# Performance work log

Measured on AMD Instinct MI355X. Metric: run time of the kernel, lower is better.

## Reference

```python
import jax, jax.numpy as jnp
import numpy as np

H = 64       # hidden size hard-coded in the module
NH = 4       # n_heads
S = 500      # stock_num
D = 10       # num_day
T = 40       # num_text (news per day)
FP = 3       # price features
FT = 512     # text embedding dim


def gru_scan(x, Wih, Whh, bih, bhh):
    """Single-sequence GRU (torch gate convention). x: (T, F) -> hidden states (T, H)."""
    gi = x @ Wih + bih  # (T, 3H) precompute input gates outside the scan

    def step(h, g):
        gh = h @ Whh + bhh
        r = jax.nn.sigmoid(g[:H] + gh[:H])
        z = jax.nn.sigmoid(g[H:2 * H] + gh[H:2 * H])
        n = jnp.tanh(g[2 * H:] + r * gh[2 * H:])
        h_new = (1.0 - z) * n + z * h
        return h_new, h_new

    h0 = jnp.zeros((H,), x.dtype)
    _, hs = jax.lax.scan(step, h0, gi)
    return hs


def attn_pool(hs, W, v):
    """Additive attention pooling over time. hs: (T, H) -> (H,)."""
    scores = jnp.tanh(hs @ W) @ v          # (T,)
    alpha = jax.nn.softmax(scores)
    return alpha @ hs


def _gru_params(key, fin, scale=0.08):
    k1, k2, k3, k4 = jax.random.split(key, 4)
    return (jax.random.normal(k1, (S, fin, 3 * H)) * scale,
            jax.random.normal(k2, (S, H, 3 * H)) * scale,
            jax.random.normal(k3, (S, 3 * H)) * scale,
            jax.random.normal(k4, (S, 3 * H)) * scale)


def _attn_params(key, scale=0.08):
    k1, k2 = jax.random.split(key)
    return (jax.random.normal(k1, (S, H, H)) * scale,
            jax.random.normal(k2, (S, H)) * scale)


def setup_inputs() -> dict:
    key = jax.random.key(0)
    ks = jax.random.split(key, 20)
    inp = {}
    inp['text_input'] = jax.random.normal(ks[0], (S, D, T, FT), dtype=jnp.float32)
    inp['price_input'] = jax.random.normal(ks[1], (S, D, FP), dtype=jnp.float32)
    inp['label'] = jax.random.randint(ks[2], (S,), 0, 2)
    inp['adj'] = jnp.ones((S, S), dtype=jnp.float32)
    inp['train'] = 0
    # per-stock stacked parameters
    (inp['Wih_p'], inp['Whh_p'], inp['bih_p'], inp['bhh_p']) = _gru_params(ks[3], FP)
    (inp['Wa_p'], inp['va_p']) = _attn_params(ks[4])
    (inp['Wih_t'], inp['Whh_t'], inp['bih_t'], inp['bhh_t']) = _gru_params(ks[5], FT)
    (inp['Wa_t'], inp['va_t']) = _attn_params(ks[6])
    (inp['Wih_s'], inp['Whh_s'], inp['bih_s'], inp['bhh_s']) = _gru_params(ks[7], H)
    (inp['Wa_s'], inp['va_s']) = _attn_params(ks[8])
    inp['Wb'] = jax.random.normal(ks[9], (S, H, H, H)) * 0.05   # Bilinear weight (out,in1,in2)
    inp['bb'] = jax.random.normal(ks[10], (S, H)) * 0.05
    inp['Wbl'] = jax.random.normal(ks[11], (S, H, 2)) * 0.08
    inp['bbl'] = jax.random.normal(ks[12], (S, 2)) * 0.08
    # shared cross-stock self-attention projections and final fc
    inp['Wq'] = jax.random.normal(ks[13], (H, H)) * 0.08
    inp['bq'] = jax.random.normal(ks[14], (H,)) * 0.08
    inp['Wk'] = jax.random.normal(ks[15], (H, H)) * 0.08
    inp['bk'] = jax.random.normal(ks[16], (H,)) * 0.08
    inp['Wf'] = jax.random.normal(ks[17], (H, 2)) * 0.08
    inp['bf'] = jax.random.normal(ks[18], (2,)) * 0.08
    return inp


def _forward(text_input, price_input, label,
             Wih_p, Whh_p, bih_p, bhh_p, Wa_p, va_p,
             Wih_t, Whh_t, bih_t, bhh_t, Wa_t, va_t,
             Wih_s, Whh_s, bih_s, bhh_s, Wa_s, va_s,
             Wb, bb, Wbl, bbl, Wq, bq, Wk, bk, Wf, bf):
    # ---- per-stock price encoder: GRU over days + attention pooling ----
    def enc_price(x, a, b, c, d, W, v):
        return attn_pool(gru_scan(x, a, b, c, d), W, v)
    x_price = jax.vmap(enc_price)(price_input, Wih_p, Whh_p, bih_p, bhh_p, Wa_p, va_p)  # (S, H)

    # ---- per-stock, per-day text encoder ----
    def enc_text_stock(xdays, a, b, c, d, W, v):
        return jax.vmap(lambda x: attn_pool(gru_scan(x, a, b, c, d), W, v))(xdays)  # (D, H)
    news = jax.vmap(enc_text_stock)(text_input, Wih_t, Whh_t, bih_t, bhh_t, Wa_t, va_t)  # (S, D, H)

    # ---- per-stock sequence encoder over days ----
    text_vec = jax.vmap(enc_price)(news, Wih_s, Whh_s, bih_s, bhh_s, Wa_s, va_s)  # (S, H)

    # ---- bilinear fusion: tanh(Bilinear(text, price)) ----
    combined = jnp.tanh(jnp.einsum('si,skij,sj->sk', text_vec, Wb, x_price) + bb)  # (S, H)

    # ---- per-stock blending head ----
    out_1 = jnp.tanh(jnp.einsum('si,sik->sk', combined, Wbl) + bbl)  # (S, 2)

    # ---- cross-stock multi-head self-attention (q,k projected, v identity) ----
    dh = H // NH
    q = (combined @ Wq + bq).reshape(S, NH, dh)
    k = (combined @ Wk + bk).reshape(S, NH, dh)
    v = combined.reshape(S, NH, dh)
    scores = jnp.einsum('shd,thd->hst', q, k) / (dh ** 0.5)
    attn = jax.nn.softmax(scores, axis=-1)
    attn_out = jnp.einsum('hst,thd->shd', attn, v).reshape(S, H)

    x = jax.nn.elu(attn_out @ Wf + bf)  # (S, 2)
    output = jax.nn.softmax(x + out_1, axis=1)
    # faithful to the original: CrossEntropyLoss applied to already-softmaxed output
    logp = jax.nn.log_softmax(output, axis=1)
    loss = -jnp.mean(logp[jnp.arange(S), label])
    return loss, output


def reference(text_input, price_input, label, adj, train,
              Wih_p, Whh_p, bih_p, bhh_p, Wa_p, va_p,
              Wih_t, Whh_t, bih_t, bhh_t, Wa_t, va_t,
              Wih_s, Whh_s, bih_s, bhh_s, Wa_s, va_s,
              Wb, bb, Wbl, bbl, Wq, bq, Wk, bk, Wf, bf):
    return _forward(text_input, price_input, label,
                    Wih_p, Whh_p, bih_p, bhh_p, Wa_p, va_p,
                    Wih_t, Whh_t, bih_t, bhh_t, Wa_t, va_t,
                    Wih_s, Whh_s, bih_s, bhh_s, Wa_s, va_s,
                    Wb, bb, Wbl, bbl, Wq, bq, Wk, bk, Wf, bf)
```

## Files before the change

### kernel.cpp

```cpp
#include <hip/hip_runtime.h>

#define Sn 500
#define Dn 10
#define Tn 40
#define FPn 3
#define FTn 512
#define Hn 64
#define G3 192
#define NHn 4

typedef __attribute__((ext_vector_type(8))) short bf8_t;
typedef __attribute__((ext_vector_type(4))) float f4_t;

__device__ __forceinline__ unsigned short f2bf(float f) {
    union { float f; unsigned int u; } v; v.f = f;
    unsigned int r = v.u + 0x7fffu + ((v.u >> 16) & 1u);
    return (unsigned short)(r >> 16);
}
__device__ __forceinline__ float bflo(unsigned int u) {
    union { unsigned int u; float f; } v; v.u = u << 16; return v.f;
}
__device__ __forceinline__ float bfhi(unsigned int u) {
    union { unsigned int u; float f; } v; v.u = u & 0xffff0000u; return v.f;
}
__device__ __forceinline__ unsigned int cvtpk(float lo, float hi) {
    unsigned int r;
    asm("v_cvt_pk_bf16_f32 %0, %1, %2" : "=v"(r) : "v"(lo), "v"(hi));
    return r;
}
__device__ __forceinline__ float sigmoidf_(float x) { return 1.f / (1.f + __expf(-x)); }
__device__ __forceinline__ float tanhf_(float x) {
    x = fminf(15.f, fmaxf(-15.f, x));
    float e = __expf(2.f * x);
    return (e - 1.f) / (e + 1.f);
}
__device__ __forceinline__ float dot8(uint4 wv, f4_t hA, f4_t hB) {
    return bflo(wv.x) * hA[0] + bfhi(wv.x) * hA[1]
         + bflo(wv.y) * hA[2] + bfhi(wv.y) * hA[3]
         + bflo(wv.z) * hB[0] + bfhi(wv.z) * hB[1]
         + bflo(wv.w) * hB[2] + bfhi(wv.w) * hB[3];
}
union bfu { bf8_t v; unsigned int u[4]; };

__global__ __launch_bounds__(64, 1) void price_gru(
    const float* __restrict__ price, const float* __restrict__ Wih_p,
    const float* __restrict__ Whh_p, const float* __restrict__ bih_p,
    const float* __restrict__ bhh_p, const float* __restrict__ Wa_p,
    const float* __restrict__ va_p, float* __restrict__ xprice)
{
    __shared__ __align__(16) unsigned char smp[33160];
    unsigned char* whh2 = smp;
    unsigned char* wa2 = smp + 24576;
    float* hbuf = (float*)(smp + 32768);
    float* priceL = (float*)(smp + 33040);

    const int s = blockIdx.x, l = threadIdx.x;
    {
        const float* W3 = Whh_p + (size_t)s * Hn * G3;
        for (int r = 0; r < 192; ++r) {
            int e = l + r * 64, i = e / G3, j = e - i * G3;
            *(unsigned short*)(whh2 + j * 128 + ((2 * i) ^ ((j & 7) << 4))) = f2bf(W3[e]);
        }
        const float* A3 = Wa_p + (size_t)s * Hn * Hn;
        for (int r = 0; r < 64; ++r) {
            int e = l + r * 64, i = e >> 6, k = e & 63;
            *(unsigned short*)(wa2 + k * 128 + ((2 * i) ^ ((k & 7) << 4))) = f2bf(A3[e]);
        }
        if (l < 30) priceL[l] = price[(size_t)s * 30 + l];
        hbuf[l] = 0.f;
        if (l < 4) hbuf[64 + l] = 0.f;
    }
    __builtin_amdgcn_wave_barrier();
    {
        float wp[3][3];
        #pragma unroll
        for (int i = 0; i < 3; ++i)
            #pragma unroll
            for (int g = 0; g < 3; ++g)
                wp[i][g] = Wih_p[(size_t)s * 3 * G3 + i * G3 + g * 64 + l];
        const float bi0 = bih_p[(size_t)s * G3 + l];
        const float bi1 = bih_p[(size_t)s * G3 + 64 + l];
        const float bi2 = bih_p[(size_t)s * G3 + 128 + l];
        const float bh0 = bhh_p[(size_t)s * G3 + l];
        const float bh1 = bhh_p[(size_t)s * G3 + 64 + l];
        const float bh2 = bhh_p[(size_t)s * G3 + 128 + l];
        const float vak = va_p[(size_t)s * Hn + l];
        const int swl = (l & 7) << 4;
        float h3 = 0.f, m3 = -1e30f, den3 = 0.f, av3 = 0.f;
        for (int t = 0; t < Dn; ++t) {
            float x0 = priceL[t * 3], x1 = priceL[t * 3 + 1], x2 = priceL[t * 3 + 2];
            float gg0 = bi0 + x0 * wp[0][0] + x1 * wp[1][0] + x2 * wp[2][0];
            float gg1 = bi1 + x0 * wp[0][1] + x1 * wp[1][1] + x2 * wp[2][1];
            float gg2 = bi2 + x0 * wp[0][2] + x1 * wp[1][2] + x2 * wp[2][2];
            float gh0 = bh0, gh1 = bh1, gh2 = bh2;
            #pragma unroll
            for (int ic = 0; ic < 8; ++ic) {
                const int off = (ic * 16) ^ swl;
                f4_t hA = *(const f4_t*)&hbuf[ic * 8];
                f4_t hB = *(const f4_t*)&hbuf[ic * 8 + 4];
                uint4 w0 = *(const uint4*)(whh2 + l * 128 + off);
                uint4 w1 = *(const uint4*)(whh2 + (l + 64) * 128 + off);
                uint4 w2 = *(const uint4*)(whh2 + (l + 128) * 128 + off);
                gh0 += dot8(w0, hA, hB); gh1 += dot8(w1, hA, hB); gh2 += dot8(w2, hA, hB);
            }
            float r = sigmoidf_(gg0 + gh0);
            float z = sigmoidf_(gg1 + gh1);
            float n = tanhf_(gg2 + r * gh2);
            h3 = (1.f - z) * n + z * h3;
            __builtin_amdgcn_wave_barrier();
            hbuf[l] = h3;
            __builtin_amdgcn_wave_barrier();
            float sk = 0.f;
            #pragma unroll
            for (int ic = 0; ic < 8; ++ic) {
                const int off = (ic * 16) ^ swl;
                uint4 wv = *(const uint4*)(wa2 + l * 128 + off);
                f4_t hA = *(const f4_t*)&hbuf[ic * 8];
                f4_t hB = *(const f4_t*)&hbuf[ic * 8 + 4];
                sk += dot8(wv, hA, hB);
            }
            float term = tanhf_(sk) * vak;
            #pragma unroll
            for (int off = 32; off; off >>= 1) term += __shfl_xor(term, off);
            float mn = fmaxf(m3, term);
            float s0 = __expf(m3 - mn);
            float p = __expf(term - mn);
            den3 = den3 * s0 + p;
            av3 = av3 * s0 + p * h3;
            m3 = mn;
        }
        xprice[(size_t)s * Hn + l] = av3 / den3;
    }
}

__global__ __launch_bounds__(256) void mega_fused(
    const float* __restrict__ text, const float* __restrict__ Wih,
    const float* __restrict__ bih, float* __restrict__ gi2,
    const float* __restrict__ Wb, const float* __restrict__ xprice,
    float* __restrict__ u)
{
    __shared__ __align__(16) unsigned char sm[20480];

    const int bid = blockIdx.x;
    const int xcd = bid & 7, ix = bid >> 3;
    const int swz = (xcd < 4 ? xcd * 813 : 3252 + (xcd - 4) * 812) + ix;
    const int grp = swz / 13, sub = swz - grp * 13;
    const int tid = threadIdx.x, w = tid >> 6, l = tid & 63;

    if (sub < 5) {
        const int s = grp, fi = sub;
        const int lr = l & 15, kg = l >> 4;
        unsigned short* Ab0 = (unsigned short*)sm;
        unsigned short* Ab1 = Ab0 + 5120;

        const float* xbase = text + ((size_t)s * 400 + fi * 80) * FTn;
        const float* Wihs = Wih + (size_t)s * FTn * G3 + w * 48 + lr;

        f4_t acc[5][3];
        #pragma unroll
        for (int a = 0; a < 5; a++)
            #pragma unroll
            for (int b = 0; b < 3; b++) acc[a][b] = (f4_t){0.f, 0.f, 0.f, 0.f};

        f4_t pa[3], pb[3];
        auto aload = [&](int kk) {
            #pragma unroll
            for (int q = 0; q < 3; ++q) {
                int c = tid + q * 256;
                if (q < 2 || tid < 128) {
                    int row = c >> 3, slot = c & 7;
                    const float* p = xbase + (size_t)row * FTn + kk * 64 + slot * 8;
                    pa[q] = *(const f4_t*)p; pb[q] = *(const f4_t*)(p + 4);
                }
            }
        };
        auto awrite = [&](unsigned short* buf) {
            #pragma unroll
            for (int q = 0; q < 3; ++q) {
                int c = tid + q * 256;
                if (q < 2 || tid < 128) {
                    int row = c >> 3, slot = c & 7;
                    uint4 uu = { cvtpk(pa[q][0], pa[q][1]), cvtpk(pa[q][2], pa[q][3]),
                                 cvtpk(pb[q][0], pb[q][1]), cvtpk(pb[q][2], pb[q][3]) };
                    *(uint4*)(buf + row * 64 + ((slot ^ (row & 7)) * 8)) = uu;
                }
            }
        };
        auto bload = [&](int kk, int ks, int nc) -> bf8_t {
            const float* bp = Wihs + (size_t)(kk * 64 + ks * 32 + kg * 8) * G3 + nc * 16;
            float b0 = bp[0], b1 = bp[G3], b2 = bp[2 * G3], b3 = bp[3 * G3];
            float b4 = bp[4 * G3], b5 = bp[5 * G3], b6 = bp[6 * G3], b7 = bp[7 * G3];
            bfu t;
            t.u[0] = cvtpk(b0, b1); t.u[1] = cvtpk(b2, b3);
            t.u[2] = cvtpk(b4, b5); t.u[3] = cvtpk(b6, b7);
            return t.v;
        };
        auto afrag = [&](const unsigned short* buf, int mt, int ks) -> bf8_t {
            int row = mt * 16 + lr;
            int slot = (ks * 4 + kg) ^ (row & 7);
            return *(const bf8_t*)(buf + row * 64 + slot * 8);
        };

        bf8_t bc[2][3], bn[2][3];
        aload(0);
        #pragma unroll
        for (int ks = 0; ks < 2; ++ks)
            #pragma unroll
            for (int nc = 0; nc < 3; ++nc) bc[ks][nc] = bload(0, ks, nc);
        awrite(Ab0);
        __syncthreads();

        for (int kk = 0; kk < 8; ++kk) {
            unsigned short* cur = (kk & 1) ? Ab1 : Ab0;
            unsigned short* nxt = (kk & 1) ? Ab0 : Ab1;
            if (kk < 7) {
                aload(kk + 1);
                #pragma unroll
                for (int ks = 0; ks < 2; ++ks)
                    #pragma unroll
                    for (int nc = 0; nc < 3; ++nc) bn[ks][nc] = bload(kk + 1, ks, nc);
            }
            #pragma unroll
            for (int ks = 0; ks < 2; ++ks)
                #pragma unroll
                for (int mt = 0; mt < 5; ++mt) {
                    bf8_t af = afrag(cur, mt, ks);
                    acc[mt][0] = __builtin_amdgcn_mfma_f32_16x16x32_bf16(af, bc[ks][0], acc[mt][0], 0, 0, 0);
                    acc[mt][1] = __builtin_amdgcn_mfma_f32_16x16x32_bf16(af, bc[ks][1], acc[mt][1], 0, 0, 0);
                    acc[mt][2] = __builtin_amdgcn_mfma_f32_16x16x32_bf16(af, bc[ks][2], acc[mt][2], 0, 0, 0);
                }
            if (kk < 7) awrite(nxt);
            __syncthreads();
            #pragma unroll
            for (int ks = 0; ks < 2; ++ks)
                #pragma unroll
                for (int nc = 0; nc < 3; ++nc) bc[ks][nc] = bn[ks][nc];
        }

        const float* bihs = bih + (size_t)s * G3 + w * 48 + lr;
        #pragma unroll
        for (int nc = 0; nc < 3; ++nc) {
            const int col = w * 48 + nc * 16 + lr;
            const float bv = bihs[nc * 16];
            #pragma unroll
            for (int mt = 0; mt < 5; ++mt)
                #pragma unroll
                for (int rg = 0; rg < 4; ++rg) {
                    int r = mt * 16 + kg * 4 + rg;
                    int hi = (r >= 40);
                    int day = fi * 2 + hi;
                    int t = r - hi * 40;
                    gi2[((size_t)(s * 40 + t) * 10 + day) * 192 + col] = acc[mt][nc][rg] + bv;
                }
        }
    } else {
        const int s = grp, kq = sub - 5;
        float* uT = (float*)sm;
        const int j4 = (l & 15) * 4;
        f4_t xq = *(const f4_t*)&xprice[s * Hn + j4];

        const float* Wbs = Wb + (size_t)s * Hn * Hn * Hn;
        for (int g = 0; g < 32; ++g) {
            int P = kq * 512 + g * 16 + w * 4 + (l >> 4);
            f4_t wv = *(const f4_t*)&Wbs[(size_t)P * Hn + j4];
            float dp = wv[0] * xq[0] + wv[1] * xq[1] + wv[2] * xq[2] + wv[3] * xq[3];
            dp += __shfl_xor(dp, 8);
            dp += __shfl_xor(dp, 4);
            dp += __shfl_xor(dp, 2);
            dp += __shfl_xor(dp, 1);
            if ((l & 15) == 0) { int k = P >> 6, i = P & 63; uT[i * 9 + (k - kq * 8)] = dp; }
        }
        __syncthreads();
        #pragma unroll
        for (int r = 0; r < 2; ++r) {
            int flat = tid + r * 256;
            int kL = flat >> 6, i = flat & 63;
            u[((size_t)s * 64 + kq * 8 + kL) * 64 + i] = uT[i * 9 + kL];
        }
    }
}

__global__ __launch_bounds__(64, 1) void gru_text_f(
    const float* __restrict__ gi2, const float* __restrict__ Whh,
    const float* __restrict__ bhh, const float* __restrict__ Wa,
    const float* __restrict__ va, float* __restrict__ news)
{
    __shared__ __align__(16) float hrow[16 * 68];
    __shared__ __align__(16) unsigned char waT[Hn * 128];

    const int s = blockIdx.x, l = threadIdx.x;
    const int lr = l & 15, lg = l >> 4;

    const float* Whhs = Whh + (size_t)s * Hn * G3;
    bfu bwhh[2][12];
    #pragma unroll
    for (int ks = 0; ks < 2; ++ks)
        #pragma unroll
        for (int nt = 0; nt < 12; ++nt) {
            const float* p = Whhs + (size_t)(ks * 32 + lg * 8) * G3 + nt * 16 + lr;
            float b0 = p[0], b1 = p[G3], b2 = p[2 * G3], b3 = p[3 * G3];
            float b4 = p[4 * G3], b5 = p[5 * G3], b6 = p[6 * G3], b7 = p[7 * G3];
            bwhh[ks][nt].u[0] = cvtpk(b0, b1); bwhh[ks][nt].u[1] = cvtpk(b2, b3);
            bwhh[ks][nt].u[2] = cvtpk(b4, b5); bwhh[ks][nt].u[3] = cvtpk(b6, b7);
        }
    float bhh_l[12];
    #pragma unroll
    for (int nt = 0; nt < 12; ++nt) bhh_l[nt] = bhh[(size_t)s * G3 + nt * 16 + lr];
    float va_l[4];
    #pragma unroll
    for (int nt = 0; nt < 4; ++nt) va_l[nt] = va[(size_t)s * Hn + nt * 16 + lr];

    {
        const float* Was = Wa + (size_t)s * Hn * Hn;
        for (int r = 0; r < 64; ++r) {
            int e = l + r * 64, i = e >> 6, k = e & 63;
            *(unsigned short*)(waT + k * 128 + ((2 * i) ^ ((k & 7) << 4))) = f2bf(Was[e]);
        }
        #pragma unroll
        for (int r = 0; r < 17; ++r) hrow[l + r * 64] = 0.f;
    }
    __builtin_amdgcn_wave_barrier();

    int dayoff[4];
    #pragma unroll
    for (int rr = 0; rr < 4; ++rr) {
        int d = lg * 4 + rr; if (d > 9) d = 9;
        dayoff[rr] = d * 192 + lr;
    }
    const float* gbase = gi2 + (size_t)s * 40 * 1920;

    float val[48], valn[48];
    #pragma unroll
    for (int j = 0; j < 48; ++j) val[j] = gbase[dayoff[j & 3] + (j >> 2) * 16];

    bf8_t a0f, a1f;
    {   bfu z0; z0.u[0] = 0; z0.u[1] = 0; z0.u[2] = 0; z0.u[3] = 0; a0f = z0.v; a1f = z0.v; }

    float h[4][4], accv[4][4], den[4], m[4];
    #pragma unroll
    for (int nt = 0; nt < 4; ++nt)
        #pragma unroll
        for (int rr = 0; rr < 4; ++rr) { h[nt][rr] = 0.f; accv[nt][rr] = 0.f; }
    #pragma unroll
    for (int rr = 0; rr < 4; ++rr) { den[rr] = 0.f; m[rr] = -1e30f; }

    for (int t = 0; t < Tn; ++t) {
        f4_t acc[12];
        #pragma unroll
        for (int nt = 0; nt < 12; ++nt)
            acc[nt] = (f4_t){bhh_l[nt], bhh_l[nt], bhh_l[nt], bhh_l[nt]};
        __builtin_amdgcn_s_setprio(1);
        #pragma unroll
        for (int nt = 0; nt < 12; ++nt) {
            acc[nt] = __builtin_amdgcn_mfma_f32_16x16x32_bf16(a0f, bwhh[0][nt].v, acc[nt], 0, 0, 0);
            acc[nt] = __builtin_amdgcn_mfma_f32_16x16x32_bf16(a1f, bwhh[1][nt].v, acc[nt], 0, 0, 0);
        }
        __builtin_amdgcn_s_setprio(0);
        {
            const int tn = (t < Tn - 1) ? t + 1 : t;
            const float* gb = gbase + (size_t)tn * 1920;
            #pragma unroll
            for (int j = 0; j < 48; ++j) valn[j] = gb[dayoff[j & 3] + (j >> 2) * 16];
        }
        #pragma unroll
        for (int nt = 0; nt < 4; ++nt)
            #pragma unroll
            for (int rr = 0; rr < 4; ++rr) {
                float r = sigmoidf_(val[nt * 4 + rr] + acc[nt][rr]);
                float z = sigmoidf_(val[(nt + 4) * 4 + rr] + acc[nt + 4][rr]);
                float n = tanhf_(val[(nt + 8) * 4 + rr] + r * acc[nt + 8][rr]);
                h[nt][rr] = (1.f - z) * n + z * h[nt][rr];
            }
        __builtin_amdgcn_wave_barrier();
        #pragma unroll
        for (int rr = 0; rr < 4; ++rr) {
            int day = lg * 4 + rr;
            if (day < Dn) {
                #pragma unroll
                for (int nt = 0; nt < 4; ++nt) hrow[day * 68 + nt * 16 + lr] = h[nt][rr];
            }
        }
        __builtin_amdgcn_wave_barrier();
        {
            const float* hp = hrow + lr * 68 + lg * 8;
            f4_t x0 = *(const f4_t*)hp,        x1 = *(const f4_t*)(hp + 4);
            f4_t y0 = *(const f4_t*)(hp + 32), y1 = *(const f4_t*)(hp + 36);
            bfu t0, t1;
            t0.u[0] = cvtpk(x0[0], x0[1]); t0.u[1] = cvtpk(x0[2], x0[3]);
            t0.u[2] = cvtpk(x1[0], x1[1]); t0.u[3] = cvtpk(x1[2], x1[3]);
            t1.u[0] = cvtpk(y0[0], y0[1]); t1.u[1] = cvtpk(y0[2], y0[3]);
            t1.u[2] = cvtpk(y1[0], y1[1]); t1.u[3] = cvtpk(y1[2], y1[3]);
            a0f = t0.v; a1f = t1.v;
        }
        f4_t sc[4];
        #pragma unroll
        for (int nt = 0; nt < 4; ++nt) sc[nt] = (f4_t){0.f, 0.f, 0.f, 0.f};
        __builtin_amdgcn_s_setprio(1);
        #pragma unroll
        for (int ks = 0; ks < 2; ++ks) {
            bf8_t av = ks ? a1f : a0f;
            #pragma unroll
            for (int nt = 0; nt < 4; ++nt) {
                bf8_t bwv = *(const bf8_t*)(waT + (nt * 16 + lr) * 128
                                            + ((ks * 64 + lg * 16) ^ ((lr & 7) << 4)));
                sc[nt] = __builtin_amdgcn_mfma_f32_16x16x32_bf16(av, bwv, sc[nt], 0, 0, 0);
            }
        }
        __builtin_amdgcn_s_setprio(0);
        float pr[4];
        #pragma unroll
        for (int rr = 0; rr < 4; ++rr) {
            pr[rr] = tanhf_(sc[0][rr]) * va_l[0] + tanhf_(sc[1][rr]) * va_l[1]
                   + tanhf_(sc[2][rr]) * va_l[2] + tanhf_(sc[3][rr]) * va_l[3];
            pr[rr] += __shfl_xor(pr[rr], 1);
            pr[rr] += __shfl_xor(pr[rr], 2);
            pr[rr] += __shfl_xor(pr[rr], 4);
            pr[rr] += __shfl_xor(pr[rr], 8);
        }
        #pragma unroll
        for (int rr = 0; rr < 4; ++rr) {
            float mn = fmaxf(m[rr], pr[rr]);
            float s0 = __expf(m[rr] - mn);
            float p = __expf(pr[rr] - mn);
            den[rr] = den[rr] * s0 + p;
            #pragma unroll
            for (int nt = 0; nt < 4; ++nt)
                accv[nt][rr] = accv[nt][rr] * s0 + p * h[nt][rr];
            m[rr] = mn;
        }
        #pragma unroll
        for (int j = 0; j < 48; ++j) val[j] = valn[j];
    }
    #pragma unroll
    for (int rr = 0; rr < 4; ++rr) {
        int day = lg * 4 + rr;
        if (day < Dn) {
            float inv = 1.f / den[rr];
            #pragma unroll
            for (int nt = 0; nt < 4; ++nt)
                news[((size_t)s * Dn + day) * Hn + nt * 16 + lr] = accv[nt][rr] * inv;
        }
    }
}

__global__ __launch_bounds__(64, 1) void day_finish(
    const float* __restrict__ news,
    const float* __restrict__ Wih_s, const float* __restrict__ Whh_s,
    const float* __restrict__ bih_s, const float* __restrict__ bhh_s,
    const float* __restrict__ Wa_s, const float* __restrict__ va_s,
    const float* __restrict__ u, const float* __restrict__ bb,
    const float* __restrict__ Wq, const float* __restrict__ bq,
    const float* __restrict__ Wk, const float* __restrict__ bk,
    const float* __restrict__ Wbl, const float* __restrict__ bbl,
    float* __restrict__ combined, float* __restrict__ qg,
    float* __restrict__ kg, float* __restrict__ out1)
{
    __shared__ __align__(16) unsigned char sm[60928];
    unsigned char* whh2 = sm;
    unsigned char* wih2 = sm + 24576;
    unsigned char* wa2 = sm + 49152;
    float* newsL = (float*)(sm + 57600);
    float* hbuf  = (float*)(sm + 60320);

    const int s = blockIdx.x, l = threadIdx.x;
    float tvv;

    {
        const float* W2 = Whh_s + (size_t)s * Hn * G3;
        const float* X2 = Wih_s + (size_t)s * Hn * G3;
        for (int r = 0; r < 192; ++r) {
            int e = l + r * 64, i = e / G3, j = e - i * G3;
            int off = j * 128 + ((2 * i) ^ ((j & 7) << 4));
            *(unsigned short*)(whh2 + off) = f2bf(W2[e]);
            *(unsigned short*)(wih2 + off) = f2bf(X2[e]);
        }
        const float* A2 = Wa_s + (size_t)s * Hn * Hn;
        for (int r = 0; r < 64; ++r) {
            int e = l + r * 64, i = e >> 6, k = e & 63;
            *(unsigned short*)(wa2 + k * 128 + ((2 * i) ^ ((k & 7) << 4))) = f2bf(A2[e]);
        }
        #pragma unroll
        for (int d = 0; d < Dn; ++d) newsL[d * 68 + l] = news[((size_t)s * Dn + d) * Hn + l];
        hbuf[l] = 0.f;
        if (l < 4) hbuf[64 + l] = 0.f;
    }
    __builtin_amdgcn_wave_barrier();
    {
        const float bi0 = bih_s[(size_t)s * G3 + l];
        const float bi1 = bih_s[(size_t)s * G3 + 64 + l];
        const float bi2 = bih_s[(size_t)s * G3 + 128 + l];
        const float bh0 = bhh_s[(size_t)s * G3 + l];
        const float bh1 = bhh_s[(size_t)s * G3 + 64 + l];
        const float bh2 = bhh_s[(size_t)s * G3 + 128 + l];
        const float vak = va_s[(size_t)s * Hn + l];
        const int swl = (l & 7) << 4;
        float h2 = 0.f, m2 = -1e30f, den2 = 0.f, av2 = 0.f;
        for (int t = 0; t < Dn; ++t) {
            float gh0 = bh0, gh1 = bh1, gh2 = bh2;
            float gg0 = bi0, gg1 = bi1, gg2 = bi2;
            #pragma unroll
            for (int ic = 0; ic < 8; ++ic) {
                const int off = (ic * 16) ^ swl;
                f4_t hA = *(const f4_t*)&hbuf[ic * 8];
                f4_t hB = *(const f4_t*)&hbuf[ic * 8 + 4];
                f4_t nA = *(const f4_t*)&newsL[t * 68 + ic * 8];
                f4_t nB = *(const f4_t*)&newsL[t * 68 + ic * 8 + 4];
                uint4 w0 = *(const uint4*)(whh2 + l * 128 + off);
                uint4 w1 = *(const uint4*)(whh2 + (l + 64) * 128 + off);
                uint4 w2 = *(const uint4*)(whh2 + (l + 128) * 128 + off);
                uint4 x0 = *(const uint4*)(wih2 + l * 128 + off);
                uint4 x1 = *(const uint4*)(wih2 + (l + 64) * 128 + off);
                uint4 x2 = *(const uint4*)(wih2 + (l + 128) * 128 + off);
                gh0 += dot8(w0, hA, hB); gh1 += dot8(w1, hA, hB); gh2 += dot8(w2, hA, hB);
                gg0 += dot8(x0, nA, nB); gg1 += dot8(x1, nA, nB); gg2 += dot8(x2, nA, nB);
            }
            float r = sigmoidf_(gg0 + gh0);
            float z = sigmoidf_(gg1 + gh1);
            float n = tanhf_(gg2 + r * gh2);
            h2 = (1.f - z) * n + z * h2;
            __builtin_amdgcn_wave_barrier();
            hbuf[l] = h2;
            __builtin_amdgcn_wave_barrier();
            float sk = 0.f;
            #pragma unroll
            for (int ic = 0; ic < 8; ++ic) {
                const int off = (ic * 16) ^ swl;
                uint4 wv = *(const uint4*)(wa2 + l * 128 + off);
                f4_t hA = *(const f4_t*)&hbuf[ic * 8];
                f4_t hB = *(const f4_t*)&hbuf[ic * 8 + 4];
                sk += dot8(wv, hA, hB);
            }
            float term = tanhf_(sk) * vak;
            #pragma unroll
            for (int off = 32; off; off >>= 1) term += __shfl_xor(term, off);
            float mn = fmaxf(m2, term);
            float s0 = __expf(m2 - mn);
            float p = __expf(term - mn);
            den2 = den2 * s0 + p;
            av2 = av2 * s0 + p * h2;
            m2 = mn;
        }
        tvv = av2 / den2;
    }
    __builtin_amdgcn_wave_barrier();

    float* uL = (float*)sm;
    float* tvL = (float*)(sm + 16640);
    float* cl  = (float*)(sm + 16960);
    tvL[l] = tvv;
    const float* ub = u + (size_t)s * 4096;
    #pragma unroll 8
    for (int i = 0; i < 64; ++i) uL[i * 65 + l] = ub[i * 64 + l];
    __builtin_amdgcn_wave_barrier();
    {
        float a = bb[s * Hn + l];
        #pragma unroll 8
        for (int i = 0; i < 64; ++i) a += tvL[i] * uL[l * 65 + i];
        float c = tanhf_(a);
        cl[l] = c;
        combined[s * Hn + l] = c;
    }
    __builtin_amdgcn_wave_barrier();
    {
        float aq = bq[l], ak = bk[l];
        for (int i = 0; i < Hn; i++) {
            float ci = cl[i];
            aq += ci * Wq[i * Hn + l];
            ak += ci * Wk[i * Hn + l];
        }
        qg[s * Hn + l] = aq; kg[s * Hn + l] = ak;
        if (l < 2) {
            float a = bbl[s * 2 + l];
            for (int i = 0; i < Hn; i++) a += cl[i] * Wbl[(size_t)s * Hn * 2 + i * 2 + l];
            out1[s * 2 + l] = tanhf_(a);
        }
    }
}

__global__ __launch_bounds__(256) void mhsa(
    const float* __restrict__ qg, const float* __restrict__ kg,
    const float* __restrict__ combined, const float* __restrict__ Wf,
    const float* __restrict__ bfp, const float* __restrict__ out1,
    float* __restrict__ dout)
{
    __shared__ __align__(16) float ql[Hn];
    __shared__ float sl[NHn][Sn];
    __shared__ float hsum[NHn];
    __shared__ float ao[Hn];
    __shared__ float red2[8];
    __shared__ float red3[4][Hn];

    const int sq = blockIdx.x, tid = threadIdx.x;
    if (tid < Hn) ql[tid] = qg[sq * Hn + tid];
    __syncthreads();

    for (int id = tid; id < Sn * NHn; id += 256) {
        int t = id >> 2, h = id & 3;
        const float* kp = &kg[t * Hn + h * 16];
        float a = 0.f;
        #pragma unroll
        for (int x = 0; x < 16; x += 4) {
            f4_t kv = *(const f4_t*)&kp[x];
            f4_t qv = *(const f4_t*)&ql[h * 16 + x];
            a += kv[0] * qv[0] + kv[1] * qv[1] + kv[2] * qv[2] + kv[3] * qv[3];
        }
        sl[h][t] = a * 0.25f;
    }
    __syncthreads();
    for (int h = 0; h < NHn; ++h) {
        float m = -1e30f;
        for (int t = tid; t < Sn; t += 256) m = fmaxf(m, sl[h][t]);
        for (int o = 32; o; o >>= 1) m = fmaxf(m, __shfl_xor(m, o));
        if ((tid & 63) == 0) red2[tid >> 6] = m;
        __syncthreads();
        m = fmaxf(fmaxf(red2[0], red2[1]), fmaxf(red2[2], red2[3]));
        float ps = 0.f;
        for (int t = tid; t < Sn; t += 256) { float p = __expf(sl[h][t] - m); sl[h][t] = p; ps += p; }
        for (int o = 32; o; o >>= 1) ps += __shfl_xor(ps, o);
        if ((tid & 63) == 0) red2[4 + (tid >> 6)] = ps;
        __syncthreads();
        if (tid == 0) hsum[h] = red2[4] + red2[5] + red2[6] + red2[7];
        __syncthreads();
    }
    {
        const int q = tid >> 6, j = tid & 63, h = j >> 4;
        float a = 0.f;
        for (int t = q * 125; t < q * 125 + 125; ++t) a += sl[h][t] * combined[t * Hn + j];
        red3[q][j] = a;
    }
    __syncthreads();
    if (tid < Hn)
        ao[tid] = (red3[0][tid] + red3[1][tid] + red3[2][tid] + red3[3][tid]) / hsum[tid >> 4];
    __syncthreads();
    if (tid == 0) {
        float l0 = bfp[0], l1 = bfp[1];
        for (int j = 0; j < Hn; j++) { float v = ao[j]; l0 += v * Wf[j * 2]; l1 += v * Wf[j * 2 + 1]; }
        l0 = l0 > 0.f ? l0 : __expf(l0) - 1.f;
        l1 = l1 > 0.f ? l1 : __expf(l1) - 1.f;
        l0 += out1[sq * 2]; l1 += out1[sq * 2 + 1];
        float m = fmaxf(l0, l1);
        float e0 = __expf(l0 - m), e1 = __expf(l1 - m);
        float inv = 1.f / (e0 + e1);
        dout[1 + sq * 2] = e0 * inv;
        dout[2 + sq * 2] = e1 * inv;
    }
}

__global__ __launch_bounds__(512) void loss_k(float* __restrict__ dout,
                                              const int* __restrict__ label)
{
    __shared__ float red[512];
    const int tid = threadIdx.x;
    float a = 0.f;
    if (tid < Sn) {
        float p0 = dout[1 + 2 * tid], p1 = dout[2 + 2 * tid];
        float m = fmaxf(p0, p1);
        float lse = m + __logf(__expf(p0 - m) + __expf(p1 - m));
        float pl = label[tid] ? p1 : p0;
        a = -(pl - lse);
    }
    red[tid] = a;
    __syncthreads();
    for (int o = 256; o; o >>= 1) {
        if (tid < o) red[tid] += red[tid + o];
        __syncthreads();
    }
    if (tid == 0) dout[0] = red[0] / (float)Sn;
}

extern "C" void kernel_launch(void* const* d_in, const int* in_sizes, int n_in,
                              void* d_out, int out_size, void* d_ws, size_t ws_size,
                              hipStream_t stream)
{
    const float* text  = (const float*)d_in[0];
    const float* price = (const float*)d_in[1];
    const int*   label = (const int*)  d_in[2];
    const float* Wih_p = (const float*)d_in[5];
    const float* Whh_p = (const float*)d_in[6];
    const float* bih_p = (const float*)d_in[7];
    const float* bhh_p = (const float*)d_in[8];
    const float* Wa_p  = (const float*)d_in[9];
    const float* va_p  = (const float*)d_in[10];
    const float* Wih_t = (const float*)d_in[11];
    const float* Whh_t = (const float*)d_in[12];
    const float* bih_t = (const float*)d_in[13];
    const float* bhh_t = (const float*)d_in[14];
    const float* Wa_t  = (const float*)d_in[15];
    const float* va_t  = (const float*)d_in[16];
    const float* Wih_s = (const float*)d_in[17];
    const float* Whh_s = (const float*)d_in[18];
    const float* bih_s = (const float*)d_in[19];
    const float* bhh_s = (const float*)d_in[20];
    const float* Wa_s  = (const float*)d_in[21];
    const float* va_s  = (const float*)d_in[22];
    const float* Wb    = (const float*)d_in[23];
    const float* bb    = (const float*)d_in[24];
    const float* Wbl   = (const float*)d_in[25];
    const float* bbl   = (const float*)d_in[26];
    const float* Wq    = (const float*)d_in[27];
    const float* bq    = (const float*)d_in[28];
    const float* Wk    = (const float*)d_in[29];
    const float* bk    = (const float*)d_in[30];
    const float* Wf    = (const float*)d_in[31];
    const float* bf_   = (const float*)d_in[32];

    float* ws = (float*)d_ws;
    float* news     = ws;
    float* xprice   = ws + 320000;
    float* combined = ws + 384000;
    float* qg       = ws + 416000;
    float* kg       = ws + 448000;
    float* out1     = ws + 480000;
    float* u        = ws + 481000;
    float* gi2      = ws + 2529000;
    float* dout = (float*)d_out;

    price_gru<<<Sn, 64, 0, stream>>>(price, Wih_p, Whh_p, bih_p, bhh_p, Wa_p, va_p, xprice);
    mega_fused<<<6500, 256, 0, stream>>>(text, Wih_t, bih_t, gi2, Wb, xprice, u);
    gru_text_f<<<Sn, 64, 0, stream>>>(gi2, Whh_t, bhh_t, Wa_t, va_t, news);
    day_finish<<<Sn, 64, 0, stream>>>(news,
                                      Wih_s, Whh_s, bih_s, bhh_s, Wa_s, va_s,
                                      u, bb, Wq, bq, Wk, bk, Wbl, bbl,
                                      combined, qg, kg, out1);
    mhsa<<<Sn, 256, 0, stream>>>(qg, kg, combined, Wf, bf_, out1, dout);
    loss_k<<<1, 512, 0, stream>>>(dout, label);
}
```

Before: 622.9 us.

## Regroup kernels: fuse text input GEMM with price GRU, bilinear with text GRU

```diff
diff --git a/kernel.cpp b/kernel.cpp
--- a/kernel.cpp
+++ b/kernel.cpp
@@ -42,19 +42,132 @@
 }
 union bfu { bf8_t v; unsigned int u[4]; };
 
-__global__ __launch_bounds__(64, 1) void price_gru(
+__global__ __launch_bounds__(256) void k1_gi_price(
+    const float* __restrict__ text, const float* __restrict__ Wih,
+    const float* __restrict__ bih, float* __restrict__ gi2,
     const float* __restrict__ price, const float* __restrict__ Wih_p,
     const float* __restrict__ Whh_p, const float* __restrict__ bih_p,
     const float* __restrict__ bhh_p, const float* __restrict__ Wa_p,
     const float* __restrict__ va_p, float* __restrict__ xprice)
 {
-    __shared__ __align__(16) unsigned char smp[33160];
-    unsigned char* whh2 = smp;
-    unsigned char* wa2 = smp + 24576;
-    float* hbuf = (float*)(smp + 32768);
-    float* priceL = (float*)(smp + 33040);
-
-    const int s = blockIdx.x, l = threadIdx.x;
+    __shared__ __align__(16) unsigned char sm[33280];
+
+    const int bid = blockIdx.x, tid = threadIdx.x;
+
+    if (bid < 2500) {
+        const int s = bid / 5, fi = bid % 5;
+        const int w = tid >> 6, l = tid & 63;
+        const int lr = l & 15, kg = l >> 4;
+        unsigned short* Asb = (unsigned short*)sm;
+        unsigned char*  Bsb = sm + 6400;
+
+        const float* xbase = text + ((size_t)s * 400 + fi * 80) * FTn;
+        const float* Wihs  = Wih + (size_t)s * FTn * G3;
+
+        f4_t acc[5][3];
+        #pragma unroll
+        for (int a = 0; a < 5; a++)
+            #pragma unroll
+            for (int b = 0; b < 3; b++) acc[a][b] = (f4_t){0.f, 0.f, 0.f, 0.f};
+
+        f4_t pa[3];
+        f4_t pb0[3], pb1[3];
+
+        auto aload = [&](int kk) {
+            #pragma unroll
+            for (int q = 0; q < 3; ++q) {
+                int t = tid + q * 256;
+                if (q < 2 || tid < 128) {
+                    int row = t >> 3, ch = t & 7;
+                    pa[q] = *(const f4_t*)(xbase + (size_t)row * FTn + kk * 32 + ch * 4);
+                }
+            }
+        };
+        auto bload = [&](int kk) {
+            #pragma unroll
+            for (int q = 0; q < 3; ++q) {
+                int t = tid + q * 256;
+                int kp = t / 48, cq = t % 48;
+                const float* p = Wihs + (size_t)(kk * 32 + 2 * kp) * G3 + cq * 4;
+                pb0[q] = *(const f4_t*)p;
+                pb1[q] = *(const f4_t*)(p + G3);
+            }
+        };
+        auto awrite = [&]() {
+            #pragma unroll
+            for (int q = 0; q < 3; ++q) {
+                int t = tid + q * 256;
+                if (q < 2 || tid < 128) {
+                    int row = t >> 3, ch = t & 7;
+                    uint2 uu = { cvtpk(pa[q][0], pa[q][1]), cvtpk(pa[q][2], pa[q][3]) };
+                    *(uint2*)((unsigned char*)Asb + row * 80 + ch * 8) = uu;
+                }
+            }
+        };
+        auto bwrite = [&]() {
+            #pragma unroll
+            for (int q = 0; q < 3; ++q) {
+                int t = tid + q * 256;
+                int kp = t / 48, cq = t % 48;
+                int base = (kp >> 2) * 3072 + (kp & 3) * 4;
+                #pragma unroll
+                for (int i = 0; i < 4; ++i) {
+                    int col = cq * 4 + i;
+                    int colp = col ^ ((col >> 2) & 7);
+                    *(unsigned int*)(Bsb + base + colp * 16) = cvtpk(pb0[q][i], pb1[q][i]);
+                }
+            }
+        };
+
+        aload(0); bload(0);
+        for (int kk = 0; kk < 16; ++kk) {
+            awrite(); bwrite();
+            __syncthreads();
+            if (kk < 15) { aload(kk + 1); bload(kk + 1); }
+            bf8_t bfr[3];
+            #pragma unroll
+            for (int nc = 0; nc < 3; ++nc) {
+                int col = w * 48 + nc * 16 + lr;
+                int colp = col ^ ((col >> 2) & 7);
+                bfr[nc] = *(const bf8_t*)(Bsb + kg * 3072 + colp * 16);
+            }
+            #pragma unroll
+            for (int mt = 0; mt < 5; ++mt) {
+                bf8_t af = *(const bf8_t*)((unsigned char*)Asb + (mt * 16 + lr) * 80 + kg * 16);
+                acc[mt][0] = __builtin_amdgcn_mfma_f32_16x16x32_bf16(af, bfr[0], acc[mt][0], 0, 0, 0);
+                acc[mt][1] = __builtin_amdgcn_mfma_f32_16x16x32_bf16(af, bfr[1], acc[mt][1], 0, 0, 0);
+                acc[mt][2] = __builtin_amdgcn_mfma_f32_16x16x32_bf16(af, bfr[2], acc[mt][2], 0, 0, 0);
+            }
+            __syncthreads();
+        }
+
+        const float* bihs = bih + (size_t)s * G3 + w * 48 + lr;
+        #pragma unroll
+        for (int nc = 0; nc < 3; ++nc) {
+            const int col = w * 48 + nc * 16 + lr;
+            const float bv = bihs[nc * 16];
+            #pragma unroll
+            for (int mt = 0; mt < 5; ++mt)
+                #pragma unroll
+                for (int rg = 0; rg < 4; ++rg) {
+                    int r = mt * 16 + kg * 4 + rg;
+                    int hi = (r >= 40);
+                    int day = fi * 2 + hi;
+                    int t = r - hi * 40;
+                    gi2[((size_t)(s * 40 + t) * 10 + day) * 192 + col] = acc[mt][nc][rg] + bv;
+                }
+        }
+        return;
+    }
+
+    const int s = bid - 2500;
+    if (tid >= 64) return;
+    const int l = tid;
+    unsigned char* whh2 = sm;
+    unsigned char* wa2 = sm + 24576;
+    float* hbuf = (float*)(sm + 32768);
+    float* priceL = (float*)(sm + 33040);
+
     {
         const float* W3 = Whh_p + (size_t)s * Hn * G3;
         for (int r = 0; r < 192; ++r) {
@@ -133,163 +246,50 @@
     }
 }
 
-__global__ __launch_bounds__(256) void mega_fused(
-    const float* __restrict__ text, const float* __restrict__ Wih,
-    const float* __restrict__ bih, float* __restrict__ gi2,
+__global__ __launch_bounds__(64, 1) void k2_text_bil(
+    const float* __restrict__ gi2, const float* __restrict__ Whh,
+    const float* __restrict__ bhh, const float* __restrict__ Wa,
+    const float* __restrict__ va, float* __restrict__ news,
     const float* __restrict__ Wb, const float* __restrict__ xprice,
     float* __restrict__ u)
 {
-    __shared__ __align__(16) unsigned char sm[20480];
-
-    const int bid = blockIdx.x;
-    const int xcd = bid & 7, ix = bid >> 3;
-    const int swz = (xcd < 4 ? xcd * 813 : 3252 + (xcd - 4) * 812) + ix;
-    const int grp = swz / 13, sub = swz - grp * 13;
-    const int tid = threadIdx.x, w = tid >> 6, l = tid & 63;
-
-    if (sub < 5) {
-        const int s = grp, fi = sub;
-        const int lr = l & 15, kg = l >> 4;
-        unsigned short* Ab0 = (unsigned short*)sm;
-        unsigned short* Ab1 = Ab0 + 5120;
-
-        const float* xbase = text + ((size_t)s * 400 + fi * 80) * FTn;
-        const float* Wihs = Wih + (size_t)s * FTn * G3 + w * 48 + lr;
-
-        f4_t acc[5][3];
-        #pragma unroll
-        for (int a = 0; a < 5; a++)
-            #pragma unroll
-            for (int b = 0; b < 3; b++) acc[a][b] = (f4_t){0.f, 0.f, 0.f, 0.f};
-
-        f4_t pa[3], pb[3];
-        auto aload = [&](int kk) {
-            #pragma unroll
-            for (int q = 0; q < 3; ++q) {
-                int c = tid + q * 256;
-                if (q < 2 || tid < 128) {
-                    int row = c >> 3, slot = c & 7;
-                    const float* p = xbase + (size_t)row * FTn + kk * 64 + slot * 8;
-                    pa[q] = *(const f4_t*)p; pb[q] = *(const f4_t*)(p + 4);
-                }
-            }
-        };
-        auto awrite = [&](unsigned short* buf) {
-            #pragma unroll
-            for (int q = 0; q < 3; ++q) {
-                int c = tid + q * 256;
-                if (q < 2 || tid < 128) {
-                    int row = c >> 3, slot = c & 7;
-                    uint4 uu = { cvtpk(pa[q][0], pa[q][1]), cvtpk(pa[q][2], pa[q][3]),
-                                 cvtpk(pb[q][0], pb[q][1]), cvtpk(pb[q][2], pb[q][3]) };
-                    *(uint4*)(buf + row * 64 + ((slot ^ (row & 7)) * 8)) = uu;
-                }
-            }
-        };
-        auto bload = [&](int kk, int ks, int nc) -> bf8_t {
-            const float* bp = Wihs + (size_t)(kk * 64 + ks * 32 + kg * 8) * G3 + nc * 16;
-            float b0 = bp[0], b1 = bp[G3], b2 = bp[2 * G3], b3 = bp[3 * G3];
-            float b4 = bp[4 * G3], b5 = bp[5 * G3], b6 = bp[6 * G3], b7 = bp[7 * G3];
-            bfu t;
-            t.u[0] = cvtpk(b0, b1); t.u[1] = cvtpk(b2, b3);
-            t.u[2] = cvtpk(b4, b5); t.u[3] = cvtpk(b6, b7);
-            return t.v;
-        };
-        auto afrag = [&](const unsigned short* buf, int mt, int ks) -> bf8_t {
-            int row = mt * 16 + lr;
-            int slot = (ks * 4 + kg) ^ (row & 7);
-            return *(const bf8_t*)(buf + row * 64 + slot * 8);
-        };
-
-        bf8_t bc[2][3], bn[2][3];
-        aload(0);
-        #pragma unroll
-        for (int ks = 0; ks < 2; ++ks)
-            #pragma unroll
-            for (int nc = 0; nc < 3; ++nc) bc[ks][nc] = bload(0, ks, nc);
-        awrite(Ab0);
-        __syncthreads();
-
-        for (int kk = 0; kk < 8; ++kk) {
-            unsigned short* cur = (kk & 1) ? Ab1 : Ab0;
-            unsigned short* nxt = (kk & 1) ? Ab0 : Ab1;
-            if (kk < 7) {
-                aload(kk + 1);
-                #pragma unroll
-                for (int ks = 0; ks < 2; ++ks)
-                    #pragma unroll
-                    for (int nc = 0; nc < 3; ++nc) bn[ks][nc] = bload(kk + 1, ks, nc);
-            }
-            #pragma unroll
-            for (int ks = 0; ks < 2; ++ks)
-                #pragma unroll
-                for (int mt = 0; mt < 5; ++mt) {
-                    bf8_t af = afrag(cur, mt, ks);
-                    acc[mt][0] = __builtin_amdgcn_mfma_f32_16x16x32_bf16(af, bc[ks][0], acc[mt][0], 0, 0, 0);
-                    acc[mt][1] = __builtin_amdgcn_mfma_f32_16x16x32_bf16(af, bc[ks][1], acc[mt][1], 0, 0, 0);
-                    acc[mt][2] = __builtin_amdgcn_mfma_f32_16x16x32_bf16(af, bc[ks][2], acc[mt][2], 0, 0, 0);
-                }
-            if (kk < 7) awrite(nxt);
-            __syncthreads();
-            #pragma unroll
-            for (int ks = 0; ks < 2; ++ks)
-                #pragma unroll
-                for (int nc = 0; nc < 3; ++nc) bc[ks][nc] = bn[ks][nc];
-        }
-
-        const float* bihs = bih + (size_t)s * G3 + w * 48 + lr;
-        #pragma unroll
-        for (int nc = 0; nc < 3; ++nc) {
-            const int col = w * 48 + nc * 16 + lr;
-            const float bv = bihs[nc * 16];
-            #pragma unroll
-            for (int mt = 0; mt < 5; ++mt)
-                #pragma unroll
-                for (int rg = 0; rg < 4; ++rg) {
-                    int r = mt * 16 + kg * 4 + rg;
-                    int hi = (r >= 40);
-                    int day = fi * 2 + hi;
-                    int t = r - hi * 40;
-                    gi2[((size_t)(s * 40 + t) * 10 + day) * 192 + col] = acc[mt][nc][rg] + bv;
-                }
-        }
-    } else {
-        const int s = grp, kq = sub - 5;
-        float* uT = (float*)sm;
+    __shared__ __align__(16) unsigned char smk[12800];
+
+    const int bid = blockIdx.x, l = threadIdx.x;
+
+    if (bid >= 500) {
+        const int idx = bid - 500;
+        const int s = idx >> 2, kq = idx & 3;
+        float* uT = (float*)smk;
         const int j4 = (l & 15) * 4;
         f4_t xq = *(const f4_t*)&xprice[s * Hn + j4];
 
         const float* Wbs = Wb + (size_t)s * Hn * Hn * Hn;
-        for (int g = 0; g < 32; ++g) {
-            int P = kq * 512 + g * 16 + w * 4 + (l >> 4);
+        #pragma unroll 4
+        for (int g = 0; g < 256; ++g) {
+            int P = kq * 1024 + g * 4 + (l >> 4);
             f4_t wv = *(const f4_t*)&Wbs[(size_t)P * Hn + j4];
             float dp = wv[0] * xq[0] + wv[1] * xq[1] + wv[2] * xq[2] + wv[3] * xq[3];
             dp += __shfl_xor(dp, 8);
             dp += __shfl_xor(dp, 4);
             dp += __shfl_xor(dp, 2);
             dp += __shfl_xor(dp, 1);
-            if ((l & 15) == 0) { int k = P >> 6, i = P & 63; uT[i * 9 + (k - kq * 8)] = dp; }
-        }
-        __syncthreads();
-        #pragma unroll
-        for (int r = 0; r < 2; ++r) {
-            int flat = tid + r * 256;
+            if ((l & 15) == 0) { int k = P >> 6, i = P & 63; uT[i * 17 + (k - kq * 16)] = dp; }
+        }
+        __builtin_amdgcn_wave_barrier();
+        #pragma unroll
+        for (int r = 0; r < 16; ++r) {
+            int flat = l + r * 64;
             int kL = flat >> 6, i = flat & 63;
-            u[((size_t)s * 64 + kq * 8 + kL) * 64 + i] = uT[i * 9 + kL];
-        }
-    }
-}
-
-__global__ __launch_bounds__(64, 1) void gru_text_f(
-    const float* __restrict__ gi2, const float* __restrict__ Whh,
-    const float* __restrict__ bhh, const float* __restrict__ Wa,
-    const float* __restrict__ va, float* __restrict__ news)
-{
-    __shared__ __align__(16) float hrow[16 * 68];
-    __shared__ __align__(16) unsigned char waT[Hn * 128];
-
-    const int s = blockIdx.x, l = threadIdx.x;
+            u[((size_t)s * 64 + kq * 16 + kL) * 64 + i] = uT[i * 17 + kL];
+        }
+        return;
+    }
+
+    const int s = bid;
     const int lr = l & 15, lg = l >> 4;
+    float* hrow = (float*)smk;
+    unsigned char* waT = smk + 4352;
 
     const float* Whhs = Whh + (size_t)s * Hn * G3;
     bfu bwhh[2][12];
@@ -383,11 +383,11 @@
         __builtin_amdgcn_wave_barrier();
         {
             const float* hp = hrow + lr * 68 + lg * 8;
-            f4_t x0 = *(const f4_t*)hp,        x1 = *(const f4_t*)(hp + 4);
+            f4_t x0 = *(const f4_t*)hp,        f4x1 = *(const f4_t*)(hp + 4);
             f4_t y0 = *(const f4_t*)(hp + 32), y1 = *(const f4_t*)(hp + 36);
             bfu t0, t1;
             t0.u[0] = cvtpk(x0[0], x0[1]); t0.u[1] = cvtpk(x0[2], x0[3]);
-            t0.u[2] = cvtpk(x1[0], x1[1]); t0.u[3] = cvtpk(x1[2], x1[3]);
+            t0.u[2] = cvtpk(f4x1[0], f4x1[1]); t0.u[3] = cvtpk(f4x1[2], f4x1[3]);
             t1.u[0] = cvtpk(y0[0], y0[1]); t1.u[1] = cvtpk(y0[2], y0[3]);
             t1.u[2] = cvtpk(y1[0], y1[1]); t1.u[3] = cvtpk(y1[2], y1[3]);
             a0f = t0.v; a1f = t1.v;
@@ -715,9 +715,11 @@
     float* gi2      = ws + 2529000;
     float* dout = (float*)d_out;
 
-    price_gru<<<Sn, 64, 0, stream>>>(price, Wih_p, Whh_p, bih_p, bhh_p, Wa_p, va_p, xprice);
-    mega_fused<<<6500, 256, 0, stream>>>(text, Wih_t, bih_t, gi2, Wb, xprice, u);
-    gru_text_f<<<Sn, 64, 0, stream>>>(gi2, Whh_t, bhh_t, Wa_t, va_t, news);
+    k1_gi_price<<<3000, 256, 0, stream>>>(text, Wih_t, bih_t, gi2,
+                                          price, Wih_p, Whh_p, bih_p, bhh_p, Wa_p, va_p,
+                                          xprice);
+    k2_text_bil<<<2500, 64, 0, stream>>>(gi2, Whh_t, bhh_t, Wa_t, va_t, news,
+                                         Wb, xprice, u);
     day_finish<<<Sn, 64, 0, stream>>>(news,
                                       Wih_s, Whh_s, bih_s, bhh_s, Wa_s, va_s,
                                       u, bb, Wq, bq, Wk, bk, Wbl, bbl,
```

Measured after the change: 797.2 us. +28.0%, slower.
